# Performance work log

Hardware: AMD Instinct MI355X
Metric: run time of the kernel (lower is better)

The kernel has to match this reference:

```python
import jax, jax.numpy as jnp
import numpy as np

N = 100000
E = 1000000
F_IN = 64
HID = 128
NCLS = 32
G = 1024
EPS = 1e-5


def setup_inputs() -> dict:
    key = jax.random.key(0)
    ks = jax.random.split(key, 6)
    x = jax.random.normal(ks[0], (N, F_IN), dtype=jnp.float32)
    edge_index = jax.random.randint(ks[1], (2, E), 0, N, dtype=jnp.int64)
    batch = jnp.sort(jax.random.randint(ks[2], (N,), 0, G, dtype=jnp.int64))
    # parameters (init per _init_weights: uniform(-0.01,0.01) linears, BN w=0.1 b=0)
    W_gcn = jax.random.uniform(ks[3], (F_IN, HID), minval=-0.01, maxval=0.01, dtype=jnp.float32)
    b_gcn = jnp.zeros((HID,), jnp.float32)
    bn1_w = jnp.full((HID,), 0.1, jnp.float32)
    bn1_b = jnp.zeros((HID,), jnp.float32)
    W_out = jax.random.uniform(ks[4], (HID, NCLS), minval=-0.01, maxval=0.01, dtype=jnp.float32)
    b_out = jnp.zeros((NCLS,), jnp.float32)
    bn2_w = jnp.full((NCLS,), 0.1, jnp.float32)
    bn2_b = jnp.zeros((NCLS,), jnp.float32)
    return {"x": x, "edge_index": edge_index, "batch": batch,
            "W_gcn": W_gcn, "b_gcn": b_gcn, "bn1_w": bn1_w, "bn1_b": bn1_b,
            "W_out": W_out, "b_out": b_out, "bn2_w": bn2_w, "bn2_b": bn2_b}


def _batchnorm(h, w, b):
    # training-mode BN: biased batch statistics over dim 0
    mu = jnp.mean(h, axis=0)
    var = jnp.var(h, axis=0)
    return (h - mu) * jax.lax.rsqrt(var + EPS) * w + b


def reference(x, edge_index, batch, W_gcn, b_gcn, bn1_w, bn1_b, W_out, b_out, bn2_w, bn2_b):
    # --- GCNConv: add self loops, symmetric norm, transform, aggregate ---
    loop = jnp.arange(N, dtype=edge_index.dtype)
    src = jnp.concatenate([edge_index[0], loop])  # [E+N]
    dst = jnp.concatenate([edge_index[1], loop])
    deg = jax.ops.segment_sum(jnp.ones_like(dst, dtype=x.dtype), dst, num_segments=N)
    dinv = jax.lax.rsqrt(deg)  # deg >= 1 thanks to self loops
    coef = dinv[src] * dinv[dst]  # [E+N]
    h = x @ W_gcn  # [N, HID] transform before gather (as PyG)
    msg = h[src] * coef[:, None]  # [E+N, HID] gathered messages
    h = jax.ops.segment_sum(msg, dst, num_segments=N) + b_gcn
    # --- BN + ReLU (dropout is identity in eval) ---
    h = jax.nn.relu(_batchnorm(h, bn1_w, bn1_b))
    # --- global_mean_pool over graphs ---
    sums = jax.ops.segment_sum(h, batch, num_segments=G)  # [G, HID]
    cnt = jax.ops.segment_sum(jnp.ones((N,), h.dtype), batch, num_segments=G)
    pooled = sums / jnp.maximum(cnt, 1.0)[:, None]
    # --- head: Linear + BN ---
    out = pooled @ W_out + b_out
    return _batchnorm(out, bn2_w, bn2_b)
```

## Files before the change

kernel.cpp:

```cpp
#include <hip/hip_runtime.h>
#include <hip/hip_fp16.h>

constexpr int N    = 100000;
constexpr int E    = 1000000;
constexpr int FIN  = 64;
constexpr int HID  = 128;
constexpr int NCLS = 32;
constexpr int G    = 1024;
constexpr float EPS = 1e-5f;

constexpr int NTILE = (N + 127) / 128;

constexpr int NBUCK = 49;
constexpr int NPB   = 2048;
constexpr int EPB   = 2048;
constexpr int CAP   = 24576;
constexpr int BIN_GRID = (E + EPB - 1) / EPB;

__global__ __launch_bounds__(256) void k_bin(const int* __restrict__ src,
                                             const int* __restrict__ dst,
                                             int* __restrict__ bucketCursor,
                                             uint2* __restrict__ bucketBuf) {
  __shared__ int bcnt[NBUCK];
  __shared__ int bscan[NBUCK];
  __shared__ int bdelta[NBUCK];
  __shared__ int lcur[NBUCK];
  __shared__ uint2 staged[EPB];
  int tid = threadIdx.x;
  int e0 = blockIdx.x * EPB;
  int cnt = E - e0 < EPB ? E - e0 : EPB;
  for (int i = tid; i < NBUCK; i += 256) bcnt[i] = 0;
  __syncthreads();
  for (int i = tid; i < cnt; i += 256) {
    int d = dst[e0 + i];
    atomicAdd(&bcnt[d >> 11], 1);
  }
  __syncthreads();
  if (tid == 0) {
    int run = 0;
    for (int b = 0; b < NBUCK; ++b) { bscan[b] = run; run += bcnt[b]; }
  }
  __syncthreads();
  if (tid < NBUCK) {
    int base = bcnt[tid] ? atomicAdd(&bucketCursor[tid], bcnt[tid]) : 0;
    bdelta[tid] = base - bscan[tid];
    lcur[tid]   = bscan[tid];
  }
  __syncthreads();
  for (int i = tid; i < cnt; i += 256) {
    int s = src[e0 + i], d = dst[e0 + i];
    int pos = atomicAdd(&lcur[d >> 11], 1);
    staged[pos] = make_uint2((unsigned)s, (unsigned)d);
  }
  __syncthreads();
  for (int i = tid; i < cnt; i += 256) {
    uint2 p = staged[i];
    int b = (int)(p.y >> 11);
    bucketBuf[(long long)b * CAP + bdelta[b] + i] = p;
  }
}

__global__ __launch_bounds__(1024) void k_build(const int* __restrict__ bucketLen,
                                                const uint2* __restrict__ bucketBuf,
                                                int* __restrict__ offsets,
                                                float* __restrict__ dinv,
                                                int* __restrict__ srclist) {
  __shared__ int cnt[NPB];
  __shared__ int part[1024];
  __shared__ int bbase;
  int b = blockIdx.x, tid = threadIdx.x;
  int n0 = b << 11;
  int nn = (N - n0 < NPB) ? (N - n0) : NPB;
  int len = bucketLen[b];
  cnt[tid] = 0; cnt[tid + 1024] = 0;
  __syncthreads();
  const uint2* buf = bucketBuf + (long long)b * CAP;
  for (int i = tid; i < len; i += 1024)
    atomicAdd(&cnt[(int)buf[i].y - n0], 1);
  if (tid == 0) {
    int s = 0;
    for (int j = 0; j < b; ++j) s += bucketLen[j];
    bbase = s;
  }
  __syncthreads();
  int c0 = cnt[2 * tid], c1 = cnt[2 * tid + 1];
  int psum = c0 + c1;
  part[tid] = psum;
  __syncthreads();
  for (int off = 1; off < 1024; off <<= 1) {
    int t = (tid >= off) ? part[tid - off] : 0;
    __syncthreads();
    part[tid] += t;
    __syncthreads();
  }
  int excl = part[tid] - psum;
  int base = bbase;
  int o0 = base + excl, o1 = base + excl + c0;
  __syncthreads();
  cnt[2 * tid] = o0; cnt[2 * tid + 1] = o1;
  if (2 * tid < nn) {
    offsets[n0 + 2 * tid] = o0;
    dinv[n0 + 2 * tid] = rsqrtf((float)c0 + 1.0f);
  }
  if (2 * tid + 1 < nn) {
    offsets[n0 + 2 * tid + 1] = o1;
    dinv[n0 + 2 * tid + 1] = rsqrtf((float)c1 + 1.0f);
  }
  if (b == NBUCK - 1 && tid == 1023) offsets[N] = base + part[1023];
  __syncthreads();
  for (int i = tid; i < len; i += 1024) {
    uint2 p = buf[i];
    int pos = atomicAdd(&cnt[(int)p.y - n0], 1);
    srclist[pos] = (int)p.x;
  }
}

__global__ void k_scale(const float4* __restrict__ x4, const float* __restrict__ dinv,
                        float2* __restrict__ y2) {
  int i = blockIdx.x * blockDim.x + threadIdx.x;
  if (i >= N * 16) return;
  int node = i >> 4;
  float c = dinv[node];
  float4 v = x4[i];
  union { float2 f; __half2 h[2]; } u;
  u.h[0] = __float22half2_rn(make_float2(v.x * c, v.y * c));
  u.h[1] = __float22half2_rn(make_float2(v.z * c, v.w * c));
  y2[i] = u.f;
}

__global__ __launch_bounds__(256) void k_gather(const int* __restrict__ offsets,
                                                const int* __restrict__ srclist,
                                                const float* __restrict__ dinv,
                                                const float2* __restrict__ y2,
                                                float4* __restrict__ agg4) {
  int node = blockIdx.x * 16 + (threadIdx.x >> 4);
  int lane = threadIdx.x & 15;
  if (node >= N) return;
  int start = offsets[node], end = offsets[node + 1];
  float cd = dinv[node];

  union { float2 f; __half2 h[2]; } u;
  float4 a0, a1, a2, a3;
  u.f = y2[node * 16 + lane];
  {
    float2 f01 = __half22float2(u.h[0]);
    float2 f23 = __half22float2(u.h[1]);
    a0 = make_float4(f01.x, f01.y, f23.x, f23.y);
  }
  a1 = make_float4(0.f, 0.f, 0.f, 0.f);
  a2 = a1; a3 = a1;

  int i = start;
  for (; i + 3 < end; i += 4) {
    int s0 = srclist[i], s1 = srclist[i + 1], s2 = srclist[i + 2], s3 = srclist[i + 3];
    union { float2 f; __half2 h[2]; } u0, u1, u2, u3;
    u0.f = y2[(long long)s0 * 16 + lane];
    u1.f = y2[(long long)s1 * 16 + lane];
    u2.f = y2[(long long)s2 * 16 + lane];
    u3.f = y2[(long long)s3 * 16 + lane];
    float2 p, q;
    p = __half22float2(u0.h[0]); q = __half22float2(u0.h[1]);
    a0.x += p.x; a0.y += p.y; a0.z += q.x; a0.w += q.y;
    p = __half22float2(u1.h[0]); q = __half22float2(u1.h[1]);
    a1.x += p.x; a1.y += p.y; a1.z += q.x; a1.w += q.y;
    p = __half22float2(u2.h[0]); q = __half22float2(u2.h[1]);
    a2.x += p.x; a2.y += p.y; a2.z += q.x; a2.w += q.y;
    p = __half22float2(u3.h[0]); q = __half22float2(u3.h[1]);
    a3.x += p.x; a3.y += p.y; a3.z += q.x; a3.w += q.y;
  }
  for (; i < end; ++i) {
    int s = srclist[i];
    u.f = y2[(long long)s * 16 + lane];
    float2 p = __half22float2(u.h[0]);
    float2 q = __half22float2(u.h[1]);
    a0.x += p.x; a0.y += p.y; a0.z += q.x; a0.w += q.y;
  }
  float4 acc;
  acc.x = ((a0.x + a1.x) + (a2.x + a3.x)) * cd;
  acc.y = ((a0.y + a1.y) + (a2.y + a3.y)) * cd;
  acc.z = ((a0.z + a1.z) + (a2.z + a3.z)) * cd;
  acc.w = ((a0.w + a1.w) + (a2.w + a3.w)) * cd;
  agg4[node * 16 + lane] = acc;
}

__global__ __launch_bounds__(256) void k_gemm2(const float* __restrict__ agg,
                                               const float* __restrict__ W,
                                               const float* __restrict__ b,
                                               float* __restrict__ h,
                                               float* __restrict__ sums) {
  __shared__ float Wl[64 * 128];
  __shared__ float rowT[64 * 128];
  int tid  = threadIdx.x;
  int row0 = blockIdx.x * 128;
  {
    const float4* Wg4 = (const float4*)W;
    float4* Wl4 = (float4*)Wl;
    for (int i = tid; i < 2048; i += 256) Wl4[i] = Wg4[i];
  }
  {
    int r = tid & 127, kh = tid >> 7;
    int grow = row0 + r;
#pragma unroll
    for (int i = 0; i < 8; ++i) {
      int k0 = kh * 32 + i * 4;
      float4 v;
      if (grow < N) v = *(const float4*)&agg[(long long)grow * 64 + k0];
      else          v = make_float4(0.f, 0.f, 0.f, 0.f);
      rowT[(k0 + 0) * 128 + r] = v.x;
      rowT[(k0 + 1) * 128 + r] = v.y;
      rowT[(k0 + 2) * 128 + r] = v.z;
      rowT[(k0 + 3) * 128 + r] = v.w;
    }
  }
  __syncthreads();

  int rt = tid >> 4, ct = tid & 15;
  float acc[8][8];
#pragma unroll
  for (int m = 0; m < 8; ++m)
#pragma unroll
    for (int j = 0; j < 8; ++j) acc[m][j] = 0.f;

#pragma unroll 4
  for (int k = 0; k < 64; ++k) {
    float4 w0 = *(const float4*)&Wl[k * 128 + ct * 8];
    float4 w1 = *(const float4*)&Wl[k * 128 + ct * 8 + 4];
    float4 r0 = *(const float4*)&rowT[k * 128 + rt * 8];
    float4 r1 = *(const float4*)&rowT[k * 128 + rt * 8 + 4];
    float wv[8] = {w0.x, w0.y, w0.z, w0.w, w1.x, w1.y, w1.z, w1.w};
    float rv[8] = {r0.x, r0.y, r0.z, r0.w, r1.x, r1.y, r1.z, r1.w};
#pragma unroll
    for (int m = 0; m < 8; ++m)
#pragma unroll
      for (int j = 0; j < 8; ++j) acc[m][j] += rv[m] * wv[j];
  }

  int cbase = ct * 8;
  float4 b0 = *(const float4*)&b[cbase];
  float4 b1 = *(const float4*)&b[cbase + 4];
  float bias[8] = {b0.x, b0.y, b0.z, b0.w, b1.x, b1.y, b1.z, b1.w};
  float s[8], s2[8];
#pragma unroll
  for (int j = 0; j < 8; ++j) { s[j] = 0.f; s2[j] = 0.f; }
#pragma unroll
  for (int m = 0; m < 8; ++m) {
    int grow = row0 + rt * 8 + m;
    if (grow < N) {
      float hv[8];
#pragma unroll
      for (int j = 0; j < 8; ++j) {
        hv[j] = acc[m][j] + bias[j];
        s[j] += hv[j];
        s2[j] += hv[j] * hv[j];
      }
      float* hp = &h[(long long)grow * 128 + cbase];
      *(float4*)hp       = make_float4(hv[0], hv[1], hv[2], hv[3]);
      *(float4*)(hp + 4) = make_float4(hv[4], hv[5], hv[6], hv[7]);
    }
  }
  __syncthreads();
  float* red = Wl;
#pragma unroll
  for (int j = 0; j < 8; ++j) {
    red[rt * 256 + cbase + j]       = s[j];
    red[rt * 256 + 128 + cbase + j] = s2[j];
  }
  __syncthreads();
  float tot = 0.f;
#pragma unroll 4
  for (int r = 0; r < 16; ++r) tot += red[r * 256 + tid];
  atomicAdd(&sums[tid], tot);
}

__global__ __launch_bounds__(128) void k_bn1_final(const float* __restrict__ sums,
                                                   const float* __restrict__ w,
                                                   const float* __restrict__ bb,
                                                   float* __restrict__ ss) {
  int tid = threadIdx.x;
  float mu  = sums[tid] * (1.0f / N);
  float var = sums[tid + 128] * (1.0f / N) - mu * mu;
  float rs  = rsqrtf(var + EPS);
  float sc  = rs * w[tid];
  ss[tid]       = sc;
  ss[tid + 128] = bb[tid] - mu * sc;
}

__global__ __launch_bounds__(256) void k_pool(const float* __restrict__ h,
                                              const float* __restrict__ ss,
                                              const int* __restrict__ batch,
                                              float* __restrict__ pooled) {
  int g = blockIdx.x;
  int lo = 0, hi = N;
  while (lo < hi) { int m = (lo + hi) >> 1; if (batch[m] < g) lo = m + 1; else hi = m; }
  int lo2 = lo, hi2 = N;
  while (lo2 < hi2) { int m = (lo2 + hi2) >> 1; if (batch[m] < g + 1) lo2 = m + 1; else hi2 = m; }
  int start = lo, end = lo2;
  int tid = threadIdx.x;
  int col = tid & 127, rp = tid >> 7;
  float sc = ss[col], sh = ss[col + 128];
  float s = 0.f;
  for (int r = start + rp; r < end; r += 2) {
    float v = h[(long long)r * 128 + col] * sc + sh;
    s += fmaxf(v, 0.f);
  }
  __shared__ float red[256];
  red[tid] = s;
  __syncthreads();
  if (tid < 128) {
    float cnt = fmaxf((float)(end - start), 1.0f);
    pooled[g * 128 + col] = (red[tid] + red[tid + 128]) / cnt;
  }
}

__global__ __launch_bounds__(256) void k_head(const float* __restrict__ pooled,
                                              const float* __restrict__ W,
                                              const float* __restrict__ b,
                                              float* __restrict__ outpre,
                                              float* __restrict__ sums2) {
  int idx = blockIdx.x * 256 + threadIdx.x;
  int g = idx >> 5, c = idx & 31;
  float acc = b[c];
  const float* pr = pooled + g * 128;
#pragma unroll
  for (int k = 0; k < 128; ++k) acc += pr[k] * W[k * 32 + c];
  outpre[idx] = acc;
  __shared__ float red[256], red2[256];
  int tid = threadIdx.x;
  red[tid] = acc; red2[tid] = acc * acc;
  __syncthreads();
  for (int off = 128; off >= 32; off >>= 1) {
    if (tid < off) { red[tid] += red[tid + off]; red2[tid] += red2[tid + off]; }
    __syncthreads();
  }
  if (tid < 32) {
    atomicAdd(&sums2[tid], red[tid]);
    atomicAdd(&sums2[tid + 32], red2[tid]);
  }
}

__global__ void k_bn2f(const float* __restrict__ sums2, const float* __restrict__ w,
                       const float* __restrict__ b, float* __restrict__ ss2) {
  int c = threadIdx.x;
  float mu  = sums2[c] * (1.0f / G);
  float var = sums2[c + 32] * (1.0f / G) - mu * mu;
  float rs  = rsqrtf(var + EPS);
  float sc  = rs * w[c];
  ss2[c]      = sc;
  ss2[c + 32] = b[c] - mu * sc;
}

__global__ void k_bn2apply(const float* __restrict__ outpre, const float* __restrict__ ss2,
                           float* __restrict__ out) {
  int idx = blockIdx.x * 256 + threadIdx.x;
  int c = idx & 31;
  out[idx] = outpre[idx] * ss2[c] + ss2[c + 32];
}

extern "C" void kernel_launch(void* const* d_in, const int* in_sizes, int n_in,
                              void* d_out, int out_size, void* d_ws, size_t ws_size,
                              hipStream_t stream) {
  const float* x   = (const float*)d_in[0];
  const int* ei    = (const int*)d_in[1];
  const int* batch = (const int*)d_in[2];
  const float* Wg  = (const float*)d_in[3];
  const float* bg  = (const float*)d_in[4];
  const float* w1  = (const float*)d_in[5];
  const float* b1  = (const float*)d_in[6];
  const float* Wo  = (const float*)d_in[7];
  const float* bo  = (const float*)d_in[8];
  const float* w2  = (const float*)d_in[9];
  const float* b2  = (const float*)d_in[10];

  float* ws     = (float*)d_ws;
  float* dinv   = ws;
  float* agg    = ws + 100352;
  float* h      = agg + (long long)N * 64;
  float* ss     = h + (long long)N * 128;
  float* sums   = ss + 256;
  float* sums2  = sums + 256;
  float* ss2    = sums2 + 64;
  float* pooled = ss2 + 64;
  float* outpre = pooled + G * 128;
  int* offsets  = (int*)(outpre + G * 32);
  int* srclist  = offsets + 100416;
  int* bucketCursor = srclist + E;
  uint2* bucketBuf = (uint2*)h;
  float2* y2       = (float2*)(h + 3000000);

  const int* src = ei;
  const int* dst = ei + E;

  hipMemsetAsync(bucketCursor, 0, 64 * sizeof(int), stream);
  hipMemsetAsync(sums, 0, (256 + 64) * sizeof(float), stream);
  k_bin<<<BIN_GRID, 256, 0, stream>>>(src, dst, bucketCursor, bucketBuf);
  k_build<<<NBUCK, 1024, 0, stream>>>(bucketCursor, bucketBuf, offsets, dinv, srclist);
  k_scale<<<(N * 16 + 255) / 256, 256, 0, stream>>>((const float4*)x, dinv, y2);
  k_gather<<<(N + 15) / 16, 256, 0, stream>>>(offsets, srclist, dinv, y2, (float4*)agg);
  k_gemm2<<<NTILE, 256, 0, stream>>>(agg, Wg, bg, h, sums);
  k_bn1_final<<<1, 128, 0, stream>>>(sums, w1, b1, ss);
  k_pool<<<G, 256, 0, stream>>>(h, ss, batch, pooled);
  k_head<<<128, 256, 0, stream>>>(pooled, Wo, bo, outpre, sums2);
  k_bn2f<<<1, 32, 0, stream>>>(sums2, w2, b2, ss2);
  k_bn2apply<<<128, 256, 0, stream>>>(outpre, ss2, (float*)d_out);
}
```

Before: 244.2 us.

## Store aggregates and hidden activations in fp16 and use fdot2 in GEMM

The gather output and the GEMM output h are now stored as packed half2 rather than fp32, which halves the memory traffic of the agg write/read and the h write/read in the pool kernel. The GEMM now runs on half2 operands with the amdgcn fdot2 instruction, accumulating in fp32, and a small prep kernel packs W into half2 pairs along K. The pool kernel is reworked to read half2 columns with four row-phases. Rounding agg, W and h to fp16 adds precision loss before BatchNorm and adds one extra tiny launch.

Result: faster. 228.7 us (-6.3%).

```diff
diff --git a/kernel.cpp b/kernel.cpp
--- a/kernel.cpp
+++ b/kernel.cpp
@@ -16,6 +16,17 @@
 constexpr int EPB   = 2048;
 constexpr int CAP   = 24576;
 constexpr int BIN_GRID = (E + EPB - 1) / EPB;
+
+typedef _Float16 half2v __attribute__((ext_vector_type(2)));
+
+__device__ inline float fdot2f(__half2 a, __half2 b, float c) {
+#if __has_builtin(__builtin_amdgcn_fdot2)
+  return __builtin_amdgcn_fdot2(*(half2v*)&a, *(half2v*)&b, c, false);
+#else
+  float2 fa = __half22float2(a), fb = __half22float2(b);
+  return c + fa.x * fb.x + fa.y * fb.y;
+#endif
+}
 
 __global__ __launch_bounds__(256) void k_bin(const int* __restrict__ src,
                                              const int* __restrict__ dst,
@@ -128,11 +139,18 @@
   y2[i] = u.f;
 }
 
+__global__ void k_wprep(const float* __restrict__ W, __half2* __restrict__ w2g) {
+  int idx = blockIdx.x * blockDim.x + threadIdx.x;
+  if (idx >= 32 * 128) return;
+  int kp = idx >> 7, col = idx & 127;
+  w2g[idx] = __floats2half2_rn(W[(2 * kp) * 128 + col], W[(2 * kp + 1) * 128 + col]);
+}
+
 __global__ __launch_bounds__(256) void k_gather(const int* __restrict__ offsets,
                                                 const int* __restrict__ srclist,
                                                 const float* __restrict__ dinv,
                                                 const float2* __restrict__ y2,
-                                                float4* __restrict__ agg4) {
+                                                float2* __restrict__ aggh) {
   int node = blockIdx.x * 16 + (threadIdx.x >> 4);
   int lane = threadIdx.x & 15;
   if (node >= N) return;
@@ -180,36 +198,40 @@
   acc.y = ((a0.y + a1.y) + (a2.y + a3.y)) * cd;
   acc.z = ((a0.z + a1.z) + (a2.z + a3.z)) * cd;
   acc.w = ((a0.w + a1.w) + (a2.w + a3.w)) * cd;
-  agg4[node * 16 + lane] = acc;
-}
-
-__global__ __launch_bounds__(256) void k_gemm2(const float* __restrict__ agg,
-                                               const float* __restrict__ W,
-                                               const float* __restrict__ b,
-                                               float* __restrict__ h,
-                                               float* __restrict__ sums) {
-  __shared__ float Wl[64 * 128];
-  __shared__ float rowT[64 * 128];
+  union { float2 f; __half2 h[2]; } o;
+  o.h[0] = __floats2half2_rn(acc.x, acc.y);
+  o.h[1] = __floats2half2_rn(acc.z, acc.w);
+  aggh[node * 16 + lane] = o.f;
+}
+
+__global__ __launch_bounds__(256) void k_gemm2h(const __half2* __restrict__ aggh2,
+                                                const __half2* __restrict__ w2g,
+                                                const float* __restrict__ b,
+                                                __half2* __restrict__ h2,
+                                                float* __restrict__ sums) {
+  __shared__ __half2 Wl[32 * 128];
+  __shared__ __half2 rowT[32 * 128];
   int tid  = threadIdx.x;
   int row0 = blockIdx.x * 128;
   {
-    const float4* Wg4 = (const float4*)W;
-    float4* Wl4 = (float4*)Wl;
-    for (int i = tid; i < 2048; i += 256) Wl4[i] = Wg4[i];
+    const float4* srcv = (const float4*)w2g;
+    float4* dstv = (float4*)Wl;
+    for (int i = tid; i < 1024; i += 256) dstv[i] = srcv[i];
   }
   {
-    int r = tid & 127, kh = tid >> 7;
+    int half = tid >> 7;
+    int r = tid & 127;
     int grow = row0 + r;
 #pragma unroll
-    for (int i = 0; i < 8; ++i) {
-      int k0 = kh * 32 + i * 4;
-      float4 v;
-      if (grow < N) v = *(const float4*)&agg[(long long)grow * 64 + k0];
-      else          v = make_float4(0.f, 0.f, 0.f, 0.f);
-      rowT[(k0 + 0) * 128 + r] = v.x;
-      rowT[(k0 + 1) * 128 + r] = v.y;
-      rowT[(k0 + 2) * 128 + r] = v.z;
-      rowT[(k0 + 3) * 128 + r] = v.w;
+    for (int c = 0; c < 4; ++c) {
+      int kp0 = half * 16 + c * 4;
+      float4 v = make_float4(0.f, 0.f, 0.f, 0.f);
+      if (grow < N) v = *(const float4*)&aggh2[(long long)grow * 32 + kp0];
+      __half2* pv = (__half2*)&v;
+      rowT[(kp0 + 0) * 128 + r] = pv[0];
+      rowT[(kp0 + 1) * 128 + r] = pv[1];
+      rowT[(kp0 + 2) * 128 + r] = pv[2];
+      rowT[(kp0 + 3) * 128 + r] = pv[3];
     }
   }
   __syncthreads();
@@ -221,18 +243,19 @@
 #pragma unroll
     for (int j = 0; j < 8; ++j) acc[m][j] = 0.f;
 
-#pragma unroll 4
-  for (int k = 0; k < 64; ++k) {
-    float4 w0 = *(const float4*)&Wl[k * 128 + ct * 8];
-    float4 w1 = *(const float4*)&Wl[k * 128 + ct * 8 + 4];
-    float4 r0 = *(const float4*)&rowT[k * 128 + rt * 8];
-    float4 r1 = *(const float4*)&rowT[k * 128 + rt * 8 + 4];
-    float wv[8] = {w0.x, w0.y, w0.z, w0.w, w1.x, w1.y, w1.z, w1.w};
-    float rv[8] = {r0.x, r0.y, r0.z, r0.w, r1.x, r1.y, r1.z, r1.w};
+#pragma unroll 2
+  for (int kp = 0; kp < 32; ++kp) {
+    float4 wv0 = *(const float4*)&Wl[kp * 128 + ct * 8];
+    float4 wv1 = *(const float4*)&Wl[kp * 128 + ct * 8 + 4];
+    float4 rv0 = *(const float4*)&rowT[kp * 128 + rt * 8];
+    float4 rv1 = *(const float4*)&rowT[kp * 128 + rt * 8 + 4];
+    __half2 wv[8], rv[8];
+    *(float4*)&wv[0] = wv0; *(float4*)&wv[4] = wv1;
+    *(float4*)&rv[0] = rv0; *(float4*)&rv[4] = rv1;
 #pragma unroll
     for (int m = 0; m < 8; ++m)
 #pragma unroll
-      for (int j = 0; j < 8; ++j) acc[m][j] += rv[m] * wv[j];
+      for (int j = 0; j < 8; ++j) acc[m][j] = fdot2f(rv[m], wv[j], acc[m][j]);
   }
 
   int cbase = ct * 8;
@@ -253,13 +276,16 @@
         s[j] += hv[j];
         s2[j] += hv[j] * hv[j];
       }
-      float* hp = &h[(long long)grow * 128 + cbase];
-      *(float4*)hp       = make_float4(hv[0], hv[1], hv[2], hv[3]);
-      *(float4*)(hp + 4) = make_float4(hv[4], hv[5], hv[6], hv[7]);
+      union { float4 f; __half2 h[4]; } o;
+      o.h[0] = __floats2half2_rn(hv[0], hv[1]);
+      o.h[1] = __floats2half2_rn(hv[2], hv[3]);
+      o.h[2] = __floats2half2_rn(hv[4], hv[5]);
+      o.h[3] = __floats2half2_rn(hv[6], hv[7]);
+      *(float4*)&h2[(long long)grow * 64 + ct * 4] = o.f;
     }
   }
   __syncthreads();
-  float* red = Wl;
+  float* red = (float*)Wl;
 #pragma unroll
   for (int j = 0; j < 8; ++j) {
     red[rt * 256 + cbase + j]       = s[j];
@@ -285,7 +311,7 @@
   ss[tid + 128] = bb[tid] - mu * sc;
 }
 
-__global__ __launch_bounds__(256) void k_pool(const float* __restrict__ h,
+__global__ __launch_bounds__(256) void k_pool(const __half2* __restrict__ h2,
                                               const float* __restrict__ ss,
                                               const int* __restrict__ batch,
                                               float* __restrict__ pooled) {
@@ -296,19 +322,24 @@
   while (lo2 < hi2) { int m = (lo2 + hi2) >> 1; if (batch[m] < g + 1) lo2 = m + 1; else hi2 = m; }
   int start = lo, end = lo2;
   int tid = threadIdx.x;
-  int col = tid & 127, rp = tid >> 7;
-  float sc = ss[col], sh = ss[col + 128];
-  float s = 0.f;
-  for (int r = start + rp; r < end; r += 2) {
-    float v = h[(long long)r * 128 + col] * sc + sh;
-    s += fmaxf(v, 0.f);
-  }
-  __shared__ float red[256];
-  red[tid] = s;
-  __syncthreads();
-  if (tid < 128) {
+  int cp = tid & 63, rp = tid >> 6;
+  float sc0 = ss[2 * cp], sc1 = ss[2 * cp + 1];
+  float sh0 = ss[2 * cp + 128], sh1 = ss[2 * cp + 129];
+  float s0 = 0.f, s1 = 0.f;
+  for (int r = start + rp; r < end; r += 4) {
+    float2 f = __half22float2(h2[(long long)r * 64 + cp]);
+    s0 += fmaxf(f.x * sc0 + sh0, 0.f);
+    s1 += fmaxf(f.y * sc1 + sh1, 0.f);
+  }
+  __shared__ float red0[256], red1[256];
+  red0[tid] = s0; red1[tid] = s1;
+  __syncthreads();
+  if (tid < 64) {
+#pragma unroll
+    for (int q = 1; q < 4; ++q) { s0 += red0[tid + q * 64]; s1 += red1[tid + q * 64]; }
     float cnt = fmaxf((float)(end - start), 1.0f);
-    pooled[g * 128 + col] = (red[tid] + red[tid + 128]) / cnt;
+    float2 o = make_float2(s0 / cnt, s1 / cnt);
+    *(float2*)&pooled[g * 128 + 2 * tid] = o;
   }
 }
 
@@ -373,9 +404,9 @@
 
   float* ws     = (float*)d_ws;
   float* dinv   = ws;
-  float* agg    = ws + 100352;
-  float* h      = agg + (long long)N * 64;
-  float* ss     = h + (long long)N * 128;
+  float* aggh_f = ws + 100352;
+  float* h2_f   = aggh_f + 1600512;
+  float* ss     = h2_f + 6400000;
   float* sums   = ss + 256;
   float* sums2  = sums + 256;
   float* ss2    = sums2 + 64;
@@ -384,21 +415,24 @@
   int* offsets  = (int*)(outpre + G * 32);
   int* srclist  = offsets + 100416;
   int* bucketCursor = srclist + E;
-  uint2* bucketBuf = (uint2*)h;
-  float2* y2       = (float2*)(h + 3000000);
+  __half2* w2g  = (__half2*)(bucketCursor + 64);
+  uint2* bucketBuf = (uint2*)h2_f;
+  float2* y2       = (float2*)(h2_f + 3100000);
 
   const int* src = ei;
   const int* dst = ei + E;
 
   hipMemsetAsync(bucketCursor, 0, 64 * sizeof(int), stream);
   hipMemsetAsync(sums, 0, (256 + 64) * sizeof(float), stream);
+  k_wprep<<<16, 256, 0, stream>>>(Wg, w2g);
   k_bin<<<BIN_GRID, 256, 0, stream>>>(src, dst, bucketCursor, bucketBuf);
   k_build<<<NBUCK, 1024, 0, stream>>>(bucketCursor, bucketBuf, offsets, dinv, srclist);
   k_scale<<<(N * 16 + 255) / 256, 256, 0, stream>>>((const float4*)x, dinv, y2);
-  k_gather<<<(N + 15) / 16, 256, 0, stream>>>(offsets, srclist, dinv, y2, (float4*)agg);
-  k_gemm2<<<NTILE, 256, 0, stream>>>(agg, Wg, bg, h, sums);
+  k_gather<<<(N + 15) / 16, 256, 0, stream>>>(offsets, srclist, dinv, y2, (float2*)aggh_f);
+  k_gemm2h<<<NTILE, 256, 0, stream>>>((const __half2*)aggh_f, w2g, bg,
+                                      (__half2*)h2_f, sums);
   k_bn1_final<<<1, 128, 0, stream>>>(sums, w1, b1, ss);
-  k_pool<<<G, 256, 0, stream>>>(h, ss, batch, pooled);
+  k_pool<<<G, 256, 0, stream>>>((const __half2*)h2_f, ss, batch, pooled);
   k_head<<<128, 256, 0, stream>>>(pooled, Wo, bo, outpre, sums2);
   k_bn2f<<<1, 32, 0, stream>>>(sums2, w2, b2, ss2);
   k_bn2apply<<<128, 256, 0, stream>>>(outpre, ss2, (float*)d_out);
```
